# Optimization experiments

Measured on AMD Instinct MI355X. Metric: run time of the kernel, lower is better.

## Reference

```python
import jax, jax.numpy as jnp
from jax import lax
import numpy as np

NUM_BLOCKS = 3
LAYERS_PER_BLOCK = 10
NUM_LAYERS = NUM_BLOCKS * LAYERS_PER_BLOCK
DILATIONS = [2 ** l for _ in range(NUM_BLOCKS) for l in range(LAYERS_PER_BLOCK)]
IN, RC, DC, SC, EC = 32, 64, 64, 64, 128
B, L = 32, 4096


def conv1d(x, w, b, dilation=1, padding=0):
    # x: [B, Cin, L], w: [Cout, Cin, K], b: [Cout]
    y = lax.conv_general_dilated(
        x, w, window_strides=(1,), padding=[(padding, padding)],
        rhs_dilation=(dilation,), dimension_numbers=('NCH', 'OIH', 'NCH'))
    return y + b[None, :, None]


def setup_inputs() -> dict:
    key = jax.random.key(0)
    ks = jax.random.split(key, 20)
    s = 0.08  # ~ kaiming scale for fan_in=128
    inp = {
        'x': jax.random.normal(ks[0], (B, L, IN), dtype=jnp.float32),
        'input_w': jax.random.normal(ks[1], (RC, IN, 1), dtype=jnp.float32) * s,
        'input_b': jnp.zeros((RC,), dtype=jnp.float32),
        'dil_w': jax.random.normal(ks[2], (NUM_LAYERS, DC, RC, 2), dtype=jnp.float32) * s,
        'dil_b': jnp.zeros((NUM_LAYERS, DC), dtype=jnp.float32),
        'gate_w': jax.random.normal(ks[3], (NUM_LAYERS, DC, RC, 2), dtype=jnp.float32) * s,
        'gate_b': jnp.zeros((NUM_LAYERS, DC), dtype=jnp.float32),
        'skip_w': jax.random.normal(ks[4], (NUM_LAYERS, SC, DC, 1), dtype=jnp.float32) * s,
        'skip_b': jnp.zeros((NUM_LAYERS, SC), dtype=jnp.float32),
        'res_w': jax.random.normal(ks[5], (NUM_LAYERS, RC, DC, 1), dtype=jnp.float32) * s,
        'res_b': jnp.zeros((NUM_LAYERS, RC), dtype=jnp.float32),
        'end1_w': jax.random.normal(ks[6], (EC, SC, 1), dtype=jnp.float32) * s,
        'end1_b': jnp.zeros((EC,), dtype=jnp.float32),
        'mean_w': jax.random.normal(ks[7], (1, EC, 1), dtype=jnp.float32) * s,
        'mean_b': jnp.zeros((1,), dtype=jnp.float32),
        'lv_w': jax.random.normal(ks[8], (1, EC, 1), dtype=jnp.float32) * s,
        'lv_b': jnp.zeros((1,), dtype=jnp.float32),
    }
    return inp


def reference(x, input_w, input_b, dil_w, dil_b, gate_w, gate_b,
              skip_w, skip_b, res_w, res_b, end1_w, end1_b,
              mean_w, mean_b, lv_w, lv_b):
    h = conv1d(jnp.transpose(x, (0, 2, 1)), input_w, input_b)  # [B, RC, L]
    skip = None
    for i in range(NUM_LAYERS):
        d = DILATIONS[i]
        # padding=d with kernel 2 -> output length L + d (faithful to torch module)
        f = jnp.tanh(conv1d(h, dil_w[i], dil_b[i], dilation=d, padding=d))
        g = jax.nn.sigmoid(conv1d(h, gate_w[i], gate_b[i], dilation=d, padding=d))
        z = f * g
        s = conv1d(z, skip_w[i], skip_b[i])
        if skip is None:
            skip = s
        else:
            m = min(skip.shape[-1], s.shape[-1])
            skip = skip[:, :, :m] + s[:, :, :m]
        r = conv1d(z, res_w[i], res_b[i])
        m = min(h.shape[-1], r.shape[-1])
        h = h[:, :, :m] + r[:, :, :m]
    y = jax.nn.relu(skip)
    y = jax.nn.relu(conv1d(y, end1_w, end1_b))
    mean_pred = conv1d(y, mean_w, mean_b)[:, :, -1]       # [B, 1]
    log_var_pred = conv1d(y, lv_w, lv_b)[:, :, -1]        # [B, 1]
    vol = jnp.exp(0.5 * log_var_pred)
    return mean_pred, log_var_pred, vol
```

## Files before the change

kernel.cpp:

```cpp
#include <hip/hip_runtime.h>
#include <hip/hip_bf16.h>
#include <cstddef>

#define L_SEQ   4096
#define BATCH   32
#define TOFF    1024
#define TBUF    3072
#define NLAYERS 30

typedef __attribute__((ext_vector_type(8))) _Float16 half8;
typedef __attribute__((ext_vector_type(4))) float f32x4;

static const size_t HSZ = (size_t)BATCH * TBUF * 64;

#define L_A  0
#define L_B  32768

__device__ inline float fast_sigmoid(float x) {
  x = fminf(fmaxf(x, -30.f), 30.f);
  return __builtin_amdgcn_rcpf(1.f + __expf(-x));
}
__device__ inline float fast_tanh(float x) {
  x = fminf(fmaxf(x, -15.f), 15.f);
  float e = __expf(-2.f * x);
  return (1.f - e) * __builtin_amdgcn_rcpf(1.f + e);
}
__device__ inline half8 lds_frag(const char* smem, int base, int row, int kk,
                                 int rowstride) {
  int byte = base + row * rowstride + kk * 2;
  byte ^= (row & 7) << 4;
  return *(const half8*)(smem + byte);
}

__global__ __launch_bounds__(256) void prep_kernel(
    const float* __restrict__ dil_w, const float* __restrict__ gate_w,
    const float* __restrict__ res_w,
    _Float16* __restrict__ W1h, _Float16* __restrict__ Wrh,
    float* __restrict__ skip_last)
{
  int idx = blockIdx.x * 256 + threadIdx.x;
  if (idx < NLAYERS * 128 * 128) {
    int l = idx >> 14, r = idx & 16383, n = r >> 7, k = r & 127;
    const float* src = (n < 64) ? dil_w : gate_w;
    int oc = n & 63;
    float v = src[(((size_t)l * 64 + oc) * 64 + (k & 63)) * 2 + (k >> 6)];
    W1h[idx] = (_Float16)v;
  }
  if (idx < NLAYERS * 64 * 64) Wrh[idx] = (_Float16)res_w[idx];
  if (idx < BATCH * 64) skip_last[idx] = 0.f;
}

__global__ __launch_bounds__(256) void input_conv_kernel(
    const float* __restrict__ x, const float* __restrict__ w,
    const float* __restrict__ bias, _Float16* __restrict__ h)
{
  __shared__ char lds[32768];
  int b = blockIdx.y;
  int t0b = 1027 + blockIdx.x * 256;
  int t = t0b + threadIdx.x;
  if (t < L_SEQ) {
    const float* xp = x + ((size_t)b * L_SEQ + t) * 32;
    float xin[32];
#pragma unroll
    for (int j = 0; j < 8; ++j) {
      float4 v = ((const float4*)xp)[j];
      xin[4*j+0] = v.x; xin[4*j+1] = v.y; xin[4*j+2] = v.z; xin[4*j+3] = v.w;
    }
#pragma unroll
    for (int q = 0; q < 8; ++q) {
      half8 pk;
#pragma unroll 2
      for (int o = 0; o < 8; ++o) {
        int oc = q * 8 + o;
        float a0 = bias[oc], a1 = 0.f;
#pragma unroll
        for (int k = 0; k < 32; k += 2) {
          a0 += w[oc * 32 + k]     * xin[k];
          a1 += w[oc * 32 + k + 1] * xin[k + 1];
        }
        pk[o] = (_Float16)(a0 + a1);
      }
      int byte = threadIdx.x * 128 + ((q ^ (threadIdx.x & 7)) * 16);
      *(half8*)(lds + byte) = pk;
    }
  }
  __syncthreads();
  _Float16* hb = h + (size_t)b * TBUF * 64;
#pragma unroll
  for (int p = 0; p < 8; ++p) {
    int B = (p * 256 + threadIdx.x) * 16;
    int row = B >> 7;
    int q = (B >> 4) & 7;
    int tg = t0b + row;
    if (tg < L_SEQ) {
      half8 v = *(const half8*)(lds + row * 128 + ((q ^ (row & 7)) * 16));
      *(half8*)(hb + (size_t)(tg - TOFF) * 64 + q * 8) = v;
    }
  }
}

__global__ __launch_bounds__(512, 4) void layer_kernel(
    const _Float16* __restrict__ hin, _Float16* __restrict__ hout,
    const _Float16* __restrict__ W1h, const _Float16* __restrict__ Wrh,
    const float* __restrict__ dil_w, const float* __restrict__ gate_w,
    const float* __restrict__ skip_w,
    const float* __restrict__ dil_b, const float* __restrict__ gate_b,
    const float* __restrict__ res_b, const float* __restrict__ skip_b,
    float* __restrict__ skip_last, int layer, int d, int tstart)
{
  extern __shared__ char smem[];
  const int b = blockIdx.y;
  const int tid = threadIdx.x;

  if (blockIdx.x == gridDim.x - 1) {
    float* hp = (float*)smem;
    float* zl = hp + 64;
    if (tid < 64)
      hp[tid] = (float)hin[((size_t)b * TBUF + (L_SEQ - d - TOFF)) * 64 + tid];
    __syncthreads();
    if (tid < 64) {
      int dc = tid;
      float f = dil_b[layer * 64 + dc], gg = gate_b[layer * 64 + dc];
      const float* wd = dil_w  + (size_t)(layer * 64 + dc) * 128;
      const float* wg = gate_w + (size_t)(layer * 64 + dc) * 128;
      for (int ic = 0; ic < 64; ++ic) {
        f  += wd[ic * 2] * hp[ic];
        gg += wg[ic * 2] * hp[ic];
      }
      zl[dc] = fast_tanh(f) * fast_sigmoid(gg);
    }
    __syncthreads();
    if (tid < 64) {
      int co = tid;
      float s = skip_b[layer * 64 + co];
      const float* wsk = skip_w + (size_t)(layer * 64 + co) * 64;
      for (int dc = 0; dc < 64; ++dc) s += wsk[dc] * zl[dc];
      skip_last[b * 64 + co] += s;
    }
    return;
  }

  const int t0 = tstart + blockIdx.x * 128;
  const _Float16* hb = hin + (size_t)b * TBUF * 64;

  {
    int row = tid >> 2, part = tid & 3;
    int t = t0 + row; if (t >= L_SEQ) t = L_SEQ - 1;
    int tsrc = (part < 2) ? (t - d) : t;
    const half8* src = (const half8*)(hb + (size_t)(tsrc - TOFF) * 64 + (part & 1) * 32);
#pragma unroll
    for (int c = 0; c < 4; ++c) {
      half8 pk = src[c];
      int byte = (row * 256 + part * 64 + c * 16) ^ ((row & 7) << 4);
      *(half8*)(smem + L_A + byte) = pk;
    }
  }
  {
    int n = tid >> 2, q = tid & 3;
    const half8* src = (const half8*)(W1h + (size_t)layer * 16384 + n * 128 + q * 32);
#pragma unroll
    for (int c = 0; c < 4; ++c) {
      half8 pk = src[c];
      int byte = (n * 256 + q * 64 + c * 16) ^ ((n & 7) << 4);
      *(half8*)(smem + L_B + byte) = pk;
    }
  }
  __syncthreads();

  const int lane = tid & 63;
  const int wv   = tid >> 6;
  const int r0   = wv * 16;
  const int lcol = lane & 15;
  const int lg   = lane >> 4;

  half8 a[4];
#pragma unroll
  for (int s = 0; s < 4; ++s)
    a[s] = lds_frag(smem, L_A, r0 + lcol, s * 32 + lg * 8, 256);
  f32x4 cf[8];
#pragma unroll
  for (int j = 0; j < 8; ++j) {
    int n = j * 16 + lcol;
    float bias = (n < 64) ? dil_b[layer * 64 + n] : gate_b[layer * 64 + n - 64];
    cf[j] = (f32x4){bias, bias, bias, bias};
  }
#pragma unroll
  for (int s = 0; s < 4; ++s) {
#pragma unroll
    for (int j = 0; j < 8; ++j) {
      half8 bb = lds_frag(smem, L_B, j * 16 + lcol, s * 32 + lg * 8, 256);
      cf[j] = __builtin_amdgcn_mfma_f32_16x16x32_f16(a[s], bb, cf[j], 0, 0, 0);
    }
  }

#pragma unroll
  for (int j = 0; j < 4; ++j) {
#pragma unroll
    for (int r = 0; r < 4; ++r) {
      float z = fast_tanh(cf[j][r]) * fast_sigmoid(cf[j + 4][r]);
      int row = r0 + lg * 4 + r;
      int byte = (row * 256 + (j * 16 + lcol) * 2) ^ ((row & 7) << 4);
      *(_Float16*)(smem + L_A + byte) = (_Float16)z;
    }
  }

  half8 wr[4][2];
  const _Float16* wrp = Wrh + (size_t)layer * 4096;
#pragma unroll
  for (int j2 = 0; j2 < 4; ++j2)
#pragma unroll
    for (int s2 = 0; s2 < 2; ++s2)
      wr[j2][s2] = *(const half8*)(wrp + (j2 * 16 + lcol) * 64 + s2 * 32 + lg * 8);

  f32x4 c2[4];
#pragma unroll
  for (int j2 = 0; j2 < 4; ++j2) {
    float bias = res_b[layer * 64 + j2 * 16 + lcol];
    c2[j2] = (f32x4){bias, bias, bias, bias};
  }
#pragma unroll
  for (int s2 = 0; s2 < 2; ++s2) {
    half8 a2 = lds_frag(smem, L_A, r0 + lcol, s2 * 32 + lg * 8, 256);
#pragma unroll
    for (int j2 = 0; j2 < 4; ++j2)
      c2[j2] = __builtin_amdgcn_mfma_f32_16x16x32_f16(a2, wr[j2][s2], c2[j2], 0, 0, 0);
  }

  __syncthreads();
#pragma unroll
  for (int j2 = 0; j2 < 4; ++j2) {
#pragma unroll
    for (int r = 0; r < 4; ++r) {
      int row = r0 + lg * 4 + r;
      int byte = (row * 256 + (j2 * 16 + lcol) * 4) ^ ((row & 7) << 4);
      *(float*)(smem + L_B + byte) = c2[j2][r];
    }
  }
  __syncthreads();

  {
    int row = tid >> 2, part = tid & 3;
    int t = t0 + row;
    if (t < L_SEQ) {
      float dl[16];
#pragma unroll
      for (int g = 0; g < 4; ++g) {
        int byte = (row * 256 + part * 64 + g * 16) ^ ((row & 7) << 4);
        float4 v = *(const float4*)(smem + L_B + byte);
        dl[4*g+0] = v.x; dl[4*g+1] = v.y; dl[4*g+2] = v.z; dl[4*g+3] = v.w;
      }
      half8 hc0 = *(const half8*)(smem + L_A +
                    ((row * 256 + 128 + part * 32) ^ ((row & 7) << 4)));
      half8 hc1 = *(const half8*)(smem + L_A +
                    ((row * 256 + 128 + part * 32 + 16) ^ ((row & 7) << 4)));
      half8 o0, o1;
#pragma unroll
      for (int e = 0; e < 8; ++e) {
        o0[e] = (_Float16)((float)hc0[e] + dl[e]);
        o1[e] = (_Float16)((float)hc1[e] + dl[8 + e]);
      }
      _Float16* dst = hout + ((size_t)b * TBUF + t - TOFF) * 64 + part * 16;
      *(half8*)dst = o0;
      *(half8*)(dst + 8) = o1;
    }
  }
}

__global__ __launch_bounds__(256) void final_kernel(
    const float* __restrict__ skip_last,
    const float* __restrict__ e1w, const float* __restrict__ e1b,
    const float* __restrict__ mw,  const float* __restrict__ mb,
    const float* __restrict__ lw,  const float* __restrict__ lb,
    float* __restrict__ out)
{
  __shared__ float rm[8][32], rl[8][32];
  int b  = threadIdx.x & 31;
  int eg = threadIdx.x >> 5;
  float y1[64];
  const float4* yp = (const float4*)(skip_last + b * 64);
#pragma unroll
  for (int q = 0; q < 16; ++q) {
    float4 v = yp[q];
    y1[4*q+0] = fmaxf(v.x, 0.f); y1[4*q+1] = fmaxf(v.y, 0.f);
    y1[4*q+2] = fmaxf(v.z, 0.f); y1[4*q+3] = fmaxf(v.w, 0.f);
  }
  float mp = 0.f, lp = 0.f;
  for (int ei = 0; ei < 16; ++ei) {
    int e = eg * 16 + ei;
    const float4* wp = (const float4*)(e1w + e * 64);
    float a0 = e1b[e], a1 = 0.f;
#pragma unroll
    for (int q = 0; q < 16; ++q) {
      float4 w4 = wp[q];
      a0 += w4.x * y1[4*q+0] + w4.z * y1[4*q+2];
      a1 += w4.y * y1[4*q+1] + w4.w * y1[4*q+3];
    }
    float a = fmaxf(a0 + a1, 0.f);
    mp += mw[e] * a;
    lp += lw[e] * a;
  }
  rm[eg][b] = mp; rl[eg][b] = lp;
  __syncthreads();
  if (threadIdx.x < 32) {
    int bb = threadIdx.x;
    float m = mb[0], l = lb[0];
#pragma unroll
    for (int g = 0; g < 8; ++g) { m += rm[g][bb]; l += rl[g][bb]; }
    out[bb]      = m;
    out[32 + bb] = l;
    out[64 + bb] = expf(0.5f * l);
  }
}

extern "C" void kernel_launch(void* const* d_in, const int* in_sizes, int n_in,
                              void* d_out, int out_size, void* d_ws, size_t ws_size,
                              hipStream_t stream)
{
  const float* x       = (const float*)d_in[0];
  const float* input_w = (const float*)d_in[1];
  const float* input_b = (const float*)d_in[2];
  const float* dil_w   = (const float*)d_in[3];
  const float* dil_b   = (const float*)d_in[4];
  const float* gate_w  = (const float*)d_in[5];
  const float* gate_b  = (const float*)d_in[6];
  const float* skip_w  = (const float*)d_in[7];
  const float* skip_b  = (const float*)d_in[8];
  const float* res_w   = (const float*)d_in[9];
  const float* res_b   = (const float*)d_in[10];
  const float* e1w     = (const float*)d_in[11];
  const float* e1b     = (const float*)d_in[12];
  const float* mw      = (const float*)d_in[13];
  const float* mb      = (const float*)d_in[14];
  const float* lw      = (const float*)d_in[15];
  const float* lb      = (const float*)d_in[16];
  float* out = (float*)d_out;

  _Float16* hA        = (_Float16*)d_ws;
  _Float16* hB        = hA + HSZ;
  float*    skip_last = (float*)(hB + HSZ);
  _Float16* W1h       = (_Float16*)(skip_last + BATCH * 64);
  _Float16* Wrh       = W1h + (size_t)NLAYERS * 128 * 128;

  int dil[NLAYERS];
  int R[NLAYERS + 1];
  for (int blk = 0; blk < 3; ++blk)
    for (int l = 0; l < 10; ++l) dil[blk * 10 + l] = 1 << l;
  R[NLAYERS] = L_SEQ;
  for (int i = NLAYERS - 1; i >= 0; --i) R[i] = R[i + 1] - dil[i];

  prep_kernel<<<(NLAYERS * 128 * 128 + 255) / 256, 256, 0, stream>>>(
      dil_w, gate_w, res_w, W1h, Wrh, skip_last);

  {
    int nt = L_SEQ - R[0];
    dim3 g((nt + 255) / 256, BATCH);
    input_conv_kernel<<<g, 256, 0, stream>>>(x, input_w, input_b, hA);
  }

  _Float16* hin  = hA;
  _Float16* hout = hB;
  for (int i = 0; i < NLAYERS; ++i) {
    int nt = L_SEQ - R[i + 1];
    dim3 g((nt + 127) / 128 + 1, BATCH);
    layer_kernel<<<g, 512, 65536, stream>>>(
        hin, hout, W1h, Wrh,
        dil_w, gate_w, skip_w,
        dil_b, gate_b, res_b, skip_b,
        skip_last, i, dil[i], R[i + 1]);
    _Float16* tmp = hin; hin = hout; hout = tmp;
  }

  final_kernel<<<1, 256, 0, stream>>>(skip_last, e1w, e1b, mw, mb, lw, lb, out);
}
```

Measured before the change: 568.1 us.

## Shrink layer tiles to 64 rows and load activations directly into registers

The layer kernel now handles 64 time rows per 256-thread block instead of 128 rows per 512 threads. Shared memory drops from 64KB to 32KB, and a single buffer is reused across phases with added barriers. The A fragments and the residual input are read straight from global memory instead of being staged in LDS, and the residual weight loads are issued earlier. The aim is higher occupancy and less LDS traffic, at the cost of twice as many blocks, each reloading the 32KB weight tile, plus more uncoalesced global reads.

Measured after the change: 655.4 us. +15.4%, slower.

```diff
diff --git a/kernel.cpp b/kernel.cpp
--- a/kernel.cpp
+++ b/kernel.cpp
@@ -13,8 +13,6 @@
 
 static const size_t HSZ = (size_t)BATCH * TBUF * 64;
 
-#define L_A  0
-#define L_B  32768
 
 __device__ inline float fast_sigmoid(float x) {
   x = fminf(fmaxf(x, -30.f), 30.f);
@@ -25,9 +23,8 @@
   float e = __expf(-2.f * x);
   return (1.f - e) * __builtin_amdgcn_rcpf(1.f + e);
 }
-__device__ inline half8 lds_frag(const char* smem, int base, int row, int kk,
-                                 int rowstride) {
-  int byte = base + row * rowstride + kk * 2;
+__device__ inline half8 lds_frag(const char* smem, int row, int kk, int rowstride) {
+  int byte = row * rowstride + kk * 2;
   byte ^= (row & 7) << 4;
   return *(const half8*)(smem + byte);
 }
@@ -99,7 +96,7 @@
   }
 }
 
-__global__ __launch_bounds__(512, 4) void layer_kernel(
+__global__ __launch_bounds__(256, 4) void layer_kernel(
     const _Float16* __restrict__ hin, _Float16* __restrict__ hout,
     const _Float16* __restrict__ W1h, const _Float16* __restrict__ Wrh,
     const float* __restrict__ dil_w, const float* __restrict__ gate_w,
@@ -140,43 +137,41 @@
     return;
   }
 
-  const int t0 = tstart + blockIdx.x * 128;
+  const int t0 = tstart + blockIdx.x * 64;
   const _Float16* hb = hin + (size_t)b * TBUF * 64;
-
-  {
-    int row = tid >> 2, part = tid & 3;
-    int t = t0 + row; if (t >= L_SEQ) t = L_SEQ - 1;
-    int tsrc = (part < 2) ? (t - d) : t;
-    const half8* src = (const half8*)(hb + (size_t)(tsrc - TOFF) * 64 + (part & 1) * 32);
-#pragma unroll
-    for (int c = 0; c < 4; ++c) {
-      half8 pk = src[c];
-      int byte = (row * 256 + part * 64 + c * 16) ^ ((row & 7) << 4);
-      *(half8*)(smem + L_A + byte) = pk;
-    }
-  }
-  {
-    int n = tid >> 2, q = tid & 3;
-    const half8* src = (const half8*)(W1h + (size_t)layer * 16384 + n * 128 + q * 32);
-#pragma unroll
-    for (int c = 0; c < 4; ++c) {
-      half8 pk = src[c];
-      int byte = (n * 256 + q * 64 + c * 16) ^ ((n & 7) << 4);
-      *(half8*)(smem + L_B + byte) = pk;
-    }
-  }
-  __syncthreads();
-
   const int lane = tid & 63;
   const int wv   = tid >> 6;
   const int r0   = wv * 16;
   const int lcol = lane & 15;
   const int lg   = lane >> 4;
 
+  int trow = t0 + r0 + lcol; if (trow >= L_SEQ) trow = L_SEQ - 1;
   half8 a[4];
 #pragma unroll
-  for (int s = 0; s < 4; ++s)
-    a[s] = lds_frag(smem, L_A, r0 + lcol, s * 32 + lg * 8, 256);
+  for (int s = 0; s < 4; ++s) {
+    int tsrc = (s < 2) ? (trow - d) : trow;
+    a[s] = *(const half8*)(hb + (size_t)(tsrc - TOFF) * 64 + (s & 1) * 32 + lg * 8);
+  }
+  half8 wr[4][2];
+  const _Float16* wrp = Wrh + (size_t)layer * 4096;
+#pragma unroll
+  for (int j2 = 0; j2 < 4; ++j2)
+#pragma unroll
+    for (int s2 = 0; s2 < 2; ++s2)
+      wr[j2][s2] = *(const half8*)(wrp + (j2 * 16 + lcol) * 64 + s2 * 32 + lg * 8);
+
+  {
+    int n = tid >> 1, half = tid & 1;
+    const half8* src = (const half8*)(W1h + (size_t)layer * 16384 + n * 128 + half * 64);
+#pragma unroll
+    for (int c = 0; c < 8; ++c) {
+      half8 pk = src[c];
+      int byte = (n * 256 + half * 128 + c * 16) ^ ((n & 7) << 4);
+      *(half8*)(smem + byte) = pk;
+    }
+  }
+  __syncthreads();
+
   f32x4 cf[8];
 #pragma unroll
   for (int j = 0; j < 8; ++j) {
@@ -188,10 +183,11 @@
   for (int s = 0; s < 4; ++s) {
 #pragma unroll
     for (int j = 0; j < 8; ++j) {
-      half8 bb = lds_frag(smem, L_B, j * 16 + lcol, s * 32 + lg * 8, 256);
+      half8 bb = lds_frag(smem, j * 16 + lcol, s * 32 + lg * 8, 256);
       cf[j] = __builtin_amdgcn_mfma_f32_16x16x32_f16(a[s], bb, cf[j], 0, 0, 0);
     }
   }
+  __syncthreads();
 
 #pragma unroll
   for (int j = 0; j < 4; ++j) {
@@ -199,18 +195,10 @@
     for (int r = 0; r < 4; ++r) {
       float z = fast_tanh(cf[j][r]) * fast_sigmoid(cf[j + 4][r]);
       int row = r0 + lg * 4 + r;
-      int byte = (row * 256 + (j * 16 + lcol) * 2) ^ ((row & 7) << 4);
-      *(_Float16*)(smem + L_A + byte) = (_Float16)z;
-    }
-  }
-
-  half8 wr[4][2];
-  const _Float16* wrp = Wrh + (size_t)layer * 4096;
-#pragma unroll
-  for (int j2 = 0; j2 < 4; ++j2)
-#pragma unroll
-    for (int s2 = 0; s2 < 2; ++s2)
-      wr[j2][s2] = *(const half8*)(wrp + (j2 * 16 + lcol) * 64 + s2 * 32 + lg * 8);
+      int byte = (row * 128 + (j * 16 + lcol) * 2) ^ ((row & 7) << 4);
+      *(_Float16*)(smem + byte) = (_Float16)z;
+    }
+  }
 
   f32x4 c2[4];
 #pragma unroll
@@ -220,24 +208,22 @@
   }
 #pragma unroll
   for (int s2 = 0; s2 < 2; ++s2) {
-    half8 a2 = lds_frag(smem, L_A, r0 + lcol, s2 * 32 + lg * 8, 256);
+    half8 a2 = lds_frag(smem, r0 + lcol, s2 * 32 + lg * 8, 128);
 #pragma unroll
     for (int j2 = 0; j2 < 4; ++j2)
       c2[j2] = __builtin_amdgcn_mfma_f32_16x16x32_f16(a2, wr[j2][s2], c2[j2], 0, 0, 0);
   }
-
-  __syncthreads();
+  __syncthreads();
+
 #pragma unroll
   for (int j2 = 0; j2 < 4; ++j2) {
 #pragma unroll
     for (int r = 0; r < 4; ++r) {
       int row = r0 + lg * 4 + r;
       int byte = (row * 256 + (j2 * 16 + lcol) * 4) ^ ((row & 7) << 4);
-      *(float*)(smem + L_B + byte) = c2[j2][r];
-    }
-  }
-  __syncthreads();
-
+      *(float*)(smem + byte) = c2[j2][r];
+    }
+  }
   {
     int row = tid >> 2, part = tid & 3;
     int t = t0 + row;
@@ -246,13 +232,12 @@
 #pragma unroll
       for (int g = 0; g < 4; ++g) {
         int byte = (row * 256 + part * 64 + g * 16) ^ ((row & 7) << 4);
-        float4 v = *(const float4*)(smem + L_B + byte);
+        float4 v = *(const float4*)(smem + byte);
         dl[4*g+0] = v.x; dl[4*g+1] = v.y; dl[4*g+2] = v.z; dl[4*g+3] = v.w;
       }
-      half8 hc0 = *(const half8*)(smem + L_A +
-                    ((row * 256 + 128 + part * 32) ^ ((row & 7) << 4)));
-      half8 hc1 = *(const half8*)(smem + L_A +
-                    ((row * 256 + 128 + part * 32 + 16) ^ ((row & 7) << 4)));
+      const _Float16* hc = hb + (size_t)(t - TOFF) * 64 + part * 16;
+      half8 hc0 = *(const half8*)hc;
+      half8 hc1 = *(const half8*)(hc + 8);
       half8 o0, o1;
 #pragma unroll
       for (int e = 0; e < 8; ++e) {
@@ -361,8 +346,8 @@
   _Float16* hout = hB;
   for (int i = 0; i < NLAYERS; ++i) {
     int nt = L_SEQ - R[i + 1];
-    dim3 g((nt + 127) / 128 + 1, BATCH);
-    layer_kernel<<<g, 512, 65536, stream>>>(
+    dim3 g((nt + 63) / 64 + 1, BATCH);
+    layer_kernel<<<g, 256, 32768, stream>>>(
         hin, hout, W1h, Wrh,
         dil_w, gate_w, skip_w,
         dil_b, gate_b, res_b, skip_b,
```
